# Kernel tuning notes

Hardware: AMD Instinct MI355X
Metric: run time of the kernel (lower is better)

The kernel has to match this reference:

```python
import jax, jax.numpy as jnp
import numpy as np

B, T, C = 2, 2048, 2048
H, D = 16, 128


def _rope(x, cos, sin):
    # x: [B,H,T,D], cos/sin: [T,D//2]
    half = x.shape[-1] // 2
    x1, x2 = x[..., :half], x[..., half:]
    c = cos[None, None, :, :]
    s = sin[None, None, :, :]
    return jnp.concatenate([x1 * c - x2 * s, x1 * s + x2 * c], axis=-1)


def setup_inputs() -> dict:
    key = jax.random.key(0)
    k1, k2, k3, k4, k5 = jax.random.split(key, 5)
    x = jax.random.normal(k1, (B, T, C), dtype=jnp.float32)
    cos = jax.random.uniform(k2, (T, D // 2), dtype=jnp.float32)
    sin = jax.random.uniform(k3, (T, D // 2), dtype=jnp.float32)
    scale = 1.0 / np.sqrt(C)
    W_qkv = jax.random.normal(k4, (C, 3 * C), dtype=jnp.float32) * scale
    W_proj = jax.random.normal(k5, (C, C), dtype=jnp.float32) * scale
    return {"x": x, "cos": cos, "sin": sin, "W_qkv": W_qkv, "W_proj": W_proj}


def reference(x, cos, sin, W_qkv, W_proj):
    Bx, Tx, Cx = x.shape
    qkv = x @ W_qkv  # [B,T,3C]
    q, k, v = jnp.split(qkv, 3, axis=-1)
    # [B,T,C] -> [B,H,T,D]
    q = q.reshape(Bx, Tx, H, D).transpose(0, 2, 1, 3)
    k = k.reshape(Bx, Tx, H, D).transpose(0, 2, 1, 3)
    v = v.reshape(Bx, Tx, H, D).transpose(0, 2, 1, 3)
    q = _rope(q, cos, sin)
    k = _rope(k, cos, sin)
    # causal SDPA
    scores = jnp.einsum("bhqd,bhkd->bhqk", q, k) / jnp.sqrt(jnp.float32(D))
    causal = jnp.tril(jnp.ones((Tx, Tx), dtype=bool))
    scores = jnp.where(causal[None, None], scores, jnp.finfo(scores.dtype).min)
    attn = jax.nn.softmax(scores, axis=-1)
    out = jnp.einsum("bhqk,bhkd->bhqd", attn, v)
    out = out.transpose(0, 2, 1, 3).reshape(Bx, Tx, Cx)
    return out @ W_proj
```

## Files before the change

### kernel.cpp

```cpp
#include <hip/hip_runtime.h>
#include <stdint.h>

#define B_  2
#define T_  2048
#define C_  2048
#define H_  16
#define D_  128
#define BH_ 32
#define M_  4096

typedef __attribute__((ext_vector_type(8))) __bf16  bf16x8;
typedef __attribute__((ext_vector_type(4))) float   floatx4;
typedef __attribute__((ext_vector_type(4))) ushort  ushortx4;

__device__ __forceinline__ ushort f2bf(float f) {
    union { float f; uint32_t u; } v; v.f = f;
    return (ushort)((v.u + 0x7fffu + ((v.u >> 16) & 1u)) >> 16);
}

__device__ __forceinline__ floatx4 mfma_bf16(bf16x8 a, bf16x8 b, floatx4 c) {
    return __builtin_amdgcn_mfma_f32_16x16x32_bf16(a, b, c, 0, 0, 0);
}

__device__ __forceinline__ void async16(const ushort* g, ushort* l) {
    __builtin_amdgcn_global_load_lds(
        (const __attribute__((address_space(1))) uint32_t*)g,
        (__attribute__((address_space(3))) uint32_t*)l, 16, 0, 0);
}

__global__ __launch_bounds__(256) void convert_bf16(
    const float* __restrict__ X, ushort* __restrict__ Xb)
{
    const int i = blockIdx.x * 256 + threadIdx.x;
    const float4 v = ((const float4*)X)[i];
    ushortx4 p = { f2bf(v.x), f2bf(v.y), f2bf(v.z), f2bf(v.w) };
    ((ushortx4*)Xb)[i] = p;
}

__global__ __launch_bounds__(256) void transpose_w(
    const float* __restrict__ W, ushort* __restrict__ Wt, int Kdim, int Ndim)
{
    __shared__ float tile[32][33];
    const int n0 = blockIdx.x * 32, k0 = blockIdx.y * 32;
    const int tx = threadIdx.x, ty = threadIdx.y;
    #pragma unroll
    for (int j = 0; j < 4; j++)
        tile[ty + j*8][tx] = W[(size_t)(k0 + ty + j*8) * Ndim + n0 + tx];
    __syncthreads();
    #pragma unroll
    for (int j = 0; j < 4; j++)
        Wt[(size_t)(n0 + ty + j*8) * Kdim + k0 + tx] = f2bf(tile[tx][ty + j*8]);
}

#define BM 128
#define BN 128
#define BK 32

__global__ __launch_bounds__(256) void gemm_bt(
    const ushort* __restrict__ A, const ushort* __restrict__ Bt,
    float* __restrict__ Co, int Ndim, int Kdim)
{
    __shared__ __align__(16) ushort As[BM * BK];
    __shared__ __align__(16) ushort Bs[BN * BK];
    const int tid  = threadIdx.x;
    const int lane = tid & 63;
    const int w    = tid >> 6;
    const int wm   = (w >> 1) * 64;
    const int wn   = (w & 1) * 64;
    const int lr   = lane & 15;
    const int quad = lane >> 4;
    const int srow = lane >> 2;
    const int soff = (lane & 3) * 8;

    const ushort* Ablk = A  + (size_t)(blockIdx.y * BM) * Kdim;
    const ushort* Bblk = Bt + (size_t)(blockIdx.x * BN) * Kdim;

    floatx4 acc[4][4];
    #pragma unroll
    for (int i = 0; i < 4; i++)
        #pragma unroll
        for (int j = 0; j < 4; j++)
            acc[i][j] = (floatx4){0.f, 0.f, 0.f, 0.f};

    for (int k0 = 0; k0 < Kdim; k0 += BK) {
        __syncthreads();
        #pragma unroll
        for (int j = 0; j < 2; j++) {
            const int row = w * 32 + j * 16 + srow;
            async16(Ablk + (size_t)row * Kdim + k0 + soff,
                    As + (w * 32 + j * 16) * BK);
            async16(Bblk + (size_t)row * Kdim + k0 + soff,
                    Bs + (w * 32 + j * 16) * BK);
        }
        __syncthreads();

        bf16x8 af[4], bfr[4];
        #pragma unroll
        for (int mi = 0; mi < 4; mi++)
            af[mi] = *(const bf16x8*)(&As[(wm + mi*16 + lr) * BK + quad * 8]);
        #pragma unroll
        for (int ni = 0; ni < 4; ni++)
            bfr[ni] = *(const bf16x8*)(&Bs[(wn + ni*16 + lr) * BK + quad * 8]);
        #pragma unroll
        for (int mi = 0; mi < 4; mi++)
            #pragma unroll
            for (int ni = 0; ni < 4; ni++)
                acc[mi][ni] = mfma_bf16(af[mi], bfr[ni], acc[mi][ni]);
    }

    const size_t row0 = (size_t)blockIdx.y * BM + wm;
    const size_t col0 = (size_t)blockIdx.x * BN + wn;
    #pragma unroll
    for (int mi = 0; mi < 4; mi++)
        #pragma unroll
        for (int ni = 0; ni < 4; ni++)
            #pragma unroll
            for (int r = 0; r < 4; r++)
                Co[(row0 + mi*16 + quad*4 + r) * (size_t)Ndim + col0 + ni*16 + lr]
                    = acc[mi][ni][r];
}

__global__ __launch_bounds__(256) void rope_qk(
    const float* __restrict__ qkv, const float* __restrict__ cosb,
    const float* __restrict__ sinb, ushort* __restrict__ qb, ushort* __restrict__ kb)
{
    const int tid = blockIdx.x * 256 + threadIdx.x;
    const int d  = tid & 63;
    const int t  = (tid >> 6) & (T_ - 1);
    const int bh = tid >> 17;
    const int b  = bh >> 4, h = bh & 15;

    const size_t base = ((size_t)(b * T_ + t)) * (3 * C_) + h * D_;
    const float c = cosb[t * 64 + d], s = sinb[t * 64 + d];
    const float q1 = qkv[base + d],       q2 = qkv[base + d + 64];
    const float k1 = qkv[base + C_ + d],  k2 = qkv[base + C_ + d + 64];

    const size_t ob = ((size_t)bh * T_ + t) * D_;
    qb[ob + d]      = f2bf(q1 * c - q2 * s);
    qb[ob + d + 64] = f2bf(q1 * s + q2 * c);
    kb[ob + d]      = f2bf(k1 * c - k2 * s);
    kb[ob + d + 64] = f2bf(k1 * s + k2 * c);
}

__global__ __launch_bounds__(256) void transpose_v(
    const float* __restrict__ qkv, ushort* __restrict__ vt)
{
    __shared__ float tile[32][33];
    const int bh = blockIdx.y;
    const int b = bh >> 4, h = bh & 15;
    const int t0 = (blockIdx.x >> 2) * 32;
    const int d0 = (blockIdx.x & 3) * 32;
    const int tx = threadIdx.x, ty = threadIdx.y;
    #pragma unroll
    for (int j = 0; j < 4; j++) {
        int t = t0 + ty + j * 8;
        tile[ty + j*8][tx] =
            qkv[((size_t)(b * T_ + t)) * (3 * C_) + 2 * C_ + h * D_ + d0 + tx];
    }
    __syncthreads();
    #pragma unroll
    for (int j = 0; j < 4; j++) {
        int d = d0 + ty + j * 8;
        vt[((size_t)bh * D_ + d) * T_ + t0 + tx] = f2bf(tile[tx][ty + j*8]);
    }
}

__global__ __launch_bounds__(256, 4) void flash_attn(
    const ushort* __restrict__ qb, const ushort* __restrict__ kb,
    const ushort* __restrict__ vt, ushort* __restrict__ attnoutb)
{
    __shared__ __align__(16) ushort kt_s[64 * 128];
    __shared__ __align__(16) ushort vt_s[128 * 64];
    __shared__ __align__(16) ushort pl_s[4][16 * 40];

    const int w    = threadIdx.x >> 6;
    const int lane = threadIdx.x & 63;
    const int lr   = lane & 15;
    const int quad = lane >> 4;

    const int bh = blockIdx.x & 31;
    const int m  = 31 - (blockIdx.x >> 5);
    const int qt = 4 * m + w;
    const int qbase = qt * 16;
    const int nk = m + 1;
    const int bb = bh >> 4, hh = bh & 15;

    const ushort* kbp = kb + (size_t)bh * T_ * D_;
    const ushort* vbp = vt + (size_t)bh * D_ * T_;
    ushort* pl = pl_s[w];

    bf16x8 qf[4];
    const ushort* qrow = qb + ((size_t)bh * T_ + qbase + lr) * D_ + quad * 8;
    #pragma unroll
    for (int kc = 0; kc < 4; kc++)
        qf[kc] = *(const bf16x8*)(qrow + kc * 32);

    floatx4 o[8];
    #pragma unroll
    for (int dc = 0; dc < 8; dc++) o[dc] = (floatx4){0.f, 0.f, 0.f, 0.f};
    floatx4 lac = (floatx4){0.f, 0.f, 0.f, 0.f};

    const __bf16 one = (__bf16)1.0f;
    const bf16x8 ones = {one, one, one, one, one, one, one, one};
    const float SCL  = 0.08838834764831845f * 1.4426950408889634f;
    const float BIAS = 23.083120654223414f;

    const int krow4 = lane >> 4;
    const int kunit = lane & 15;
    const int vrow8 = lane >> 3;
    const int vunit = lane & 7;

    for (int kt = 0; kt < nk; ++kt) {
        const int kb0 = kt * 64;
        __syncthreads();
        #pragma unroll
        for (int j = 0; j < 4; j++) {
            const int row = w * 16 + j * 4 + krow4;
            const ushort* gp = kbp + (size_t)(kb0 + row) * D_
                                   + ((kunit ^ (row & 15)) << 3);
            async16(gp, kt_s + (w * 16 + j * 4) * 128);
        }
        #pragma unroll
        for (int j = 0; j < 4; j++) {
            const int row = w * 32 + j * 8 + vrow8;
            const ushort* gp = vbp + (size_t)row * T_ + kb0
                                   + ((vunit ^ (row & 7)) << 3);
            async16(gp, vt_s + (w * 32 + j * 8) * 64);
        }
        __syncthreads();

        #pragma unroll
        for (int half = 0; half < 2; ++half) {
            floatx4 st[2];
            #pragma unroll
            for (int jj = 0; jj < 2; ++jj) {
                const int j = half * 2 + jj;
                floatx4 s = (floatx4){0.f, 0.f, 0.f, 0.f};
                const int kl = j * 16 + lr;
                #pragma unroll
                for (int kc = 0; kc < 4; kc++) {
                    bf16x8 af = *(const bf16x8*)(
                        kt_s + kl * 128 + ((((kc << 2) | quad) ^ lr) << 3));
                    s = mfma_bf16(af, qf[kc], s);
                }
                st[jj] = s;
            }
            #pragma unroll
            for (int jj = 0; jj < 2; ++jj) {
                const int j = half * 2 + jj;
                const int kg0 = kb0 + j * 16 + quad * 4;
                float p[4];
                #pragma unroll
                for (int r = 0; r < 4; r++) {
                    float e = __builtin_amdgcn_exp2f(fmaf(st[jj][r], SCL, -BIAS));
                    p[r] = (kg0 + r > qbase + lr) ? 0.f : e;
                }
                uint2 pk;
                pk.x = (uint32_t)f2bf(p[0]) | ((uint32_t)f2bf(p[1]) << 16);
                pk.y = (uint32_t)f2bf(p[2]) | ((uint32_t)f2bf(p[3]) << 16);
                *(uint2*)(pl + lr * 40 + jj * 16 + quad * 4) = pk;
            }
            bf16x8 pf = *(const bf16x8*)(pl + lr * 40 + quad * 8);
            lac = mfma_bf16(pf, ones, lac);
            #pragma unroll
            for (int dc = 0; dc < 8; dc++) {
                const int d = dc * 16 + lr;
                bf16x8 vf = *(const bf16x8*)(
                    vt_s + d * 64 + ((((half << 2) | quad) ^ (lr & 7)) << 3));
                o[dc] = mfma_bf16(pf, vf, o[dc]);
            }
        }
    }

    #pragma unroll
    for (int dc = 0; dc < 8; dc++)
        #pragma unroll
        for (int r = 0; r < 4; r++) {
            const int trow = qbase + quad * 4 + r;
            attnoutb[((size_t)(bb * T_ + trow)) * C_ + hh * D_ + dc * 16 + lr]
                = f2bf(o[dc][r] / lac[r]);
        }
}

extern "C" void kernel_launch(void* const* d_in, const int* in_sizes, int n_in,
                              void* d_out, int out_size, void* d_ws, size_t ws_size,
                              hipStream_t stream)
{
    (void)in_sizes; (void)n_in; (void)out_size; (void)ws_size;
    const float* x     = (const float*)d_in[0];
    const float* cosb  = (const float*)d_in[1];
    const float* sinb  = (const float*)d_in[2];
    const float* Wqkv  = (const float*)d_in[3];
    const float* Wproj = (const float*)d_in[4];
    float* out = (float*)d_out;

    char* ws = (char*)d_ws;
    float*  qkv      = (float*)(ws);
    ushort* attnoutb = (ushort*)(ws);
    ushort* Wtq = (ushort*)(ws + 100663296);
    ushort* qb  = (ushort*)(ws + 100663296);
    ushort* Wtp = (ushort*)(ws + 125829120);
    ushort* kbf = (ushort*)(ws + 134217728);
    ushort* vt  = (ushort*)(ws + 150994944);
    ushort* xb  = (ushort*)(ws + 167772160);

    dim3 tb32(32, 8);
    transpose_w<<<dim3(3 * C_ / 32, C_ / 32), tb32, 0, stream>>>(Wqkv, Wtq, C_, 3 * C_);
    transpose_w<<<dim3(C_ / 32, C_ / 32),     tb32, 0, stream>>>(Wproj, Wtp, C_, C_);
    convert_bf16<<<(M_ * C_ / 4) / 256, 256, 0, stream>>>(x, xb);

    gemm_bt<<<dim3(3 * C_ / BN, M_ / BM), 256, 0, stream>>>(xb, Wtq, qkv, 3 * C_, C_);

    rope_qk<<<(BH_ * T_ * 64) / 256, 256, 0, stream>>>(qkv, cosb, sinb, qb, kbf);
    transpose_v<<<dim3((T_ / 32) * (D_ / 32), BH_), tb32, 0, stream>>>(qkv, vt);

    flash_attn<<<BH_ * 32, 256, 0, stream>>>(qb, kbf, vt, attnoutb);

    gemm_bt<<<dim3(C_ / BN, M_ / BM), 256, 0, stream>>>(attnoutb, Wtp, out, C_, C_);
}
```

Baseline: 427.0 us.

## Fuse RoPE and V transpose into QKV GEMM epilogue

Replaces the fp32 QKV GEMM output plus separate rope_qk and transpose_v kernels with a GEMM whose epilogue stages the 128x128 tile in LDS. Q and K tiles get RoPE applied and are written as bf16, and V tiles are written transposed through a swizzled LDS layout. This removes the write and re-read of a large fp32 qkv buffer and two kernel launches. The trade-off is an extra bf16 rounding before RoPE is applied and a heavier, branchy epilogue.

```diff
diff --git a/kernel.cpp b/kernel.cpp
--- a/kernel.cpp
+++ b/kernel.cpp
@@ -16,6 +16,11 @@
 __device__ __forceinline__ ushort f2bf(float f) {
     union { float f; uint32_t u; } v; v.f = f;
     return (ushort)((v.u + 0x7fffu + ((v.u >> 16) & 1u)) >> 16);
+}
+
+__device__ __forceinline__ float bf2f(ushort u) {
+    union { uint32_t u; float f; } v; v.u = ((uint32_t)u) << 16;
+    return v.f;
 }
 
 __device__ __forceinline__ floatx4 mfma_bf16(bf16x8 a, bf16x8 b, floatx4 c) {
@@ -120,48 +125,139 @@
                     = acc[mi][ni][r];
 }
 
-__global__ __launch_bounds__(256) void rope_qk(
-    const float* __restrict__ qkv, const float* __restrict__ cosb,
-    const float* __restrict__ sinb, ushort* __restrict__ qb, ushort* __restrict__ kb)
-{
-    const int tid = blockIdx.x * 256 + threadIdx.x;
-    const int d  = tid & 63;
-    const int t  = (tid >> 6) & (T_ - 1);
-    const int bh = tid >> 17;
-    const int b  = bh >> 4, h = bh & 15;
-
-    const size_t base = ((size_t)(b * T_ + t)) * (3 * C_) + h * D_;
-    const float c = cosb[t * 64 + d], s = sinb[t * 64 + d];
-    const float q1 = qkv[base + d],       q2 = qkv[base + d + 64];
-    const float k1 = qkv[base + C_ + d],  k2 = qkv[base + C_ + d + 64];
-
-    const size_t ob = ((size_t)bh * T_ + t) * D_;
-    qb[ob + d]      = f2bf(q1 * c - q2 * s);
-    qb[ob + d + 64] = f2bf(q1 * s + q2 * c);
-    kb[ob + d]      = f2bf(k1 * c - k2 * s);
-    kb[ob + d + 64] = f2bf(k1 * s + k2 * c);
-}
-
-__global__ __launch_bounds__(256) void transpose_v(
-    const float* __restrict__ qkv, ushort* __restrict__ vt)
-{
-    __shared__ float tile[32][33];
-    const int bh = blockIdx.y;
-    const int b = bh >> 4, h = bh & 15;
-    const int t0 = (blockIdx.x >> 2) * 32;
-    const int d0 = (blockIdx.x & 3) * 32;
-    const int tx = threadIdx.x, ty = threadIdx.y;
-    #pragma unroll
-    for (int j = 0; j < 4; j++) {
-        int t = t0 + ty + j * 8;
-        tile[ty + j*8][tx] =
-            qkv[((size_t)(b * T_ + t)) * (3 * C_) + 2 * C_ + h * D_ + d0 + tx];
+__global__ __launch_bounds__(256) void gemm_qkv(
+    const ushort* __restrict__ A, const ushort* __restrict__ Bt,
+    const float* __restrict__ cosb, const float* __restrict__ sinb,
+    ushort* __restrict__ qb, ushort* __restrict__ kbf, ushort* __restrict__ vt)
+{
+    __shared__ __align__(16) ushort smem[17408];
+    ushort* As = smem;
+    ushort* Bs = smem + 4096;
+
+    const int tid  = threadIdx.x;
+    const int lane = tid & 63;
+    const int w    = tid >> 6;
+    const int wm   = (w >> 1) * 64;
+    const int wn   = (w & 1) * 64;
+    const int lr   = lane & 15;
+    const int quad = lane >> 4;
+    const int srow = lane >> 2;
+    const int soff = (lane & 3) * 8;
+
+    const int Kdim = C_;
+    const ushort* Ablk = A  + (size_t)(blockIdx.y * BM) * Kdim;
+    const ushort* Bblk = Bt + (size_t)(blockIdx.x * BN) * Kdim;
+
+    floatx4 acc[4][4];
+    #pragma unroll
+    for (int i = 0; i < 4; i++)
+        #pragma unroll
+        for (int j = 0; j < 4; j++)
+            acc[i][j] = (floatx4){0.f, 0.f, 0.f, 0.f};
+
+    for (int k0 = 0; k0 < Kdim; k0 += BK) {
+        __syncthreads();
+        #pragma unroll
+        for (int j = 0; j < 2; j++) {
+            const int row = w * 32 + j * 16 + srow;
+            async16(Ablk + (size_t)row * Kdim + k0 + soff,
+                    As + (w * 32 + j * 16) * BK);
+            async16(Bblk + (size_t)row * Kdim + k0 + soff,
+                    Bs + (w * 32 + j * 16) * BK);
+        }
+        __syncthreads();
+
+        bf16x8 af[4], bfr[4];
+        #pragma unroll
+        for (int mi = 0; mi < 4; mi++)
+            af[mi] = *(const bf16x8*)(&As[(wm + mi*16 + lr) * BK + quad * 8]);
+        #pragma unroll
+        for (int ni = 0; ni < 4; ni++)
+            bfr[ni] = *(const bf16x8*)(&Bs[(wn + ni*16 + lr) * BK + quad * 8]);
+        #pragma unroll
+        for (int mi = 0; mi < 4; mi++)
+            #pragma unroll
+            for (int ni = 0; ni < 4; ni++)
+                acc[mi][ni] = mfma_bf16(af[mi], bfr[ni], acc[mi][ni]);
     }
+
+    const int h   = blockIdx.x & 15;
+    const int qt  = blockIdx.x >> 4;
+    const int b   = blockIdx.y >> 4;
+    const int t0g = (blockIdx.y & 15) * 128;
+    const int bh  = b * 16 + h;
+
     __syncthreads();
-    #pragma unroll
-    for (int j = 0; j < 4; j++) {
-        int d = d0 + ty + j * 8;
-        vt[((size_t)bh * D_ + d) * T_ + t0 + tx] = f2bf(tile[tx][ty + j*8]);
+
+    if (qt < 2) {
+        #pragma unroll
+        for (int mi = 0; mi < 4; mi++)
+            #pragma unroll
+            for (int ni = 0; ni < 4; ni++)
+                #pragma unroll
+                for (int r = 0; r < 4; r++) {
+                    const int t = wm + mi*16 + quad*4 + r;
+                    const int d = wn + ni*16 + lr;
+                    smem[t * 136 + d] = f2bf(acc[mi][ni][r]);
+                }
+        __syncthreads();
+
+        const int t  = tid >> 1;
+        const int c0 = (tid & 1) * 32;
+        bf16x8 x1v[4], x2v[4];
+        #pragma unroll
+        for (int u = 0; u < 4; u++) {
+            x1v[u] = *(const bf16x8*)(smem + t * 136 + c0 + u * 8);
+            x2v[u] = *(const bf16x8*)(smem + t * 136 + 64 + c0 + u * 8);
+        }
+        const float4* cp4 = (const float4*)(cosb + (size_t)(t0g + t) * 64 + c0);
+        const float4* sp4 = (const float4*)(sinb + (size_t)(t0g + t) * 64 + c0);
+        ushort* outp = (qt == 0 ? qb : kbf) + ((size_t)bh * T_ + t0g + t) * D_;
+        #pragma unroll
+        for (int u = 0; u < 4; u++) {
+            float cc[8], ss[8];
+            *(float4*)(cc)     = cp4[u * 2];
+            *(float4*)(cc + 4) = cp4[u * 2 + 1];
+            *(float4*)(ss)     = sp4[u * 2];
+            *(float4*)(ss + 4) = sp4[u * 2 + 1];
+            ushortx4 lo0, lo1, hi0, hi1;
+            #pragma unroll
+            for (int e = 0; e < 8; e++) {
+                const float x1 = (float)x1v[u][e];
+                const float x2 = (float)x2v[u][e];
+                const ushort vlo = f2bf(x1 * cc[e] - x2 * ss[e]);
+                const ushort vhi = f2bf(x1 * ss[e] + x2 * cc[e]);
+                if (e < 4) { lo0[e] = vlo; hi0[e] = vhi; }
+                else       { lo1[e-4] = vlo; hi1[e-4] = vhi; }
+            }
+            *(ushortx4*)(outp + c0 + u*8)          = lo0;
+            *(ushortx4*)(outp + c0 + u*8 + 4)      = lo1;
+            *(ushortx4*)(outp + 64 + c0 + u*8)     = hi0;
+            *(ushortx4*)(outp + 64 + c0 + u*8 + 4) = hi1;
+        }
+    } else {
+        #pragma unroll
+        for (int mi = 0; mi < 4; mi++)
+            #pragma unroll
+            for (int ni = 0; ni < 4; ni++)
+                #pragma unroll
+                for (int r = 0; r < 4; r++) {
+                    const int t = wm + mi*16 + quad*4 + r;
+                    const int d = wn + ni*16 + lr;
+                    smem[d * 128 + (t & 7) + 8 * ((t >> 3) ^ (d & 15))]
+                        = f2bf(acc[mi][ni][r]);
+                }
+        __syncthreads();
+
+        const int d    = tid >> 1;
+        const int half = tid & 1;
+        ushort* outp = vt + ((size_t)bh * D_ + d) * T_ + t0g + half * 64;
+        #pragma unroll
+        for (int u = 0; u < 8; u++) {
+            const int gu = half * 8 + u;
+            bf16x8 vv = *(const bf16x8*)(smem + d * 128 + 8 * (gu ^ (d & 15)));
+            *(bf16x8*)(outp + u * 8) = vv;
+        }
     }
 }
 
@@ -295,24 +391,21 @@
     float* out = (float*)d_out;
 
     char* ws = (char*)d_ws;
-    float*  qkv      = (float*)(ws);
-    ushort* attnoutb = (ushort*)(ws);
-    ushort* Wtq = (ushort*)(ws + 100663296);
-    ushort* qb  = (ushort*)(ws + 100663296);
-    ushort* Wtp = (ushort*)(ws + 125829120);
-    ushort* kbf = (ushort*)(ws + 134217728);
-    ushort* vt  = (ushort*)(ws + 150994944);
-    ushort* xb  = (ushort*)(ws + 167772160);
+    ushort* xb       = (ushort*)(ws);
+    ushort* Wtq      = (ushort*)(ws + 16777216);
+    ushort* Wtp      = (ushort*)(ws + 41943040);
+    ushort* qb       = (ushort*)(ws + 50331648);
+    ushort* kbf      = (ushort*)(ws + 67108864);
+    ushort* vt       = (ushort*)(ws + 83886080);
+    ushort* attnoutb = (ushort*)(ws + 100663296);
 
     dim3 tb32(32, 8);
     transpose_w<<<dim3(3 * C_ / 32, C_ / 32), tb32, 0, stream>>>(Wqkv, Wtq, C_, 3 * C_);
     transpose_w<<<dim3(C_ / 32, C_ / 32),     tb32, 0, stream>>>(Wproj, Wtp, C_, C_);
     convert_bf16<<<(M_ * C_ / 4) / 256, 256, 0, stream>>>(x, xb);
 
-    gemm_bt<<<dim3(3 * C_ / BN, M_ / BM), 256, 0, stream>>>(xb, Wtq, qkv, 3 * C_, C_);
-
-    rope_qk<<<(BH_ * T_ * 64) / 256, 256, 0, stream>>>(qkv, cosb, sinb, qb, kbf);
-    transpose_v<<<dim3((T_ / 32) * (D_ / 32), BH_), tb32, 0, stream>>>(qkv, vt);
+    gemm_qkv<<<dim3(3 * C_ / BN, M_ / BM), 256, 0, stream>>>(
+        xb, Wtq, cosb, sinb, qb, kbf, vt);
 
     flash_attn<<<BH_ * 32, 256, 0, stream>>>(qb, kbf, vt, attnoutb);
 
```

Result: faster. 407.5 us (-4.6%).
